# Optimization experiments

Measured on AMD Instinct MI355X. Metric: run time of the kernel, lower is better.

Reference implementation:

```python
import jax, jax.numpy as jnp
import numpy as np

B = 64        # graphs per batch
H = 8         # heads
EH = 16       # each_head = ceil(128/8)
HD = 128      # h_dimension
N_DA = 100000
N_Q = 20000
E_DA = 1000000
E_Q = 200000
EPS = 1e-5    # BatchNorm1d eps
SLOPE = 2.0   # leaky_relu_GAT_rate


def setup_inputs() -> dict:
    key = jax.random.key(0)
    ks = jax.random.split(key, 24)
    r = lambda i, shape, s=1.0: jax.random.normal(ks[i], shape, dtype=jnp.float32) * s
    return {
        'h_da_last': r(0, (N_DA, HD)),
        'h_q_last': r(1, (N_Q, HD)),
        'h_da_0': r(2, (N_DA, HD)),
        'h_q_0': r(3, (N_Q, HD)),
        'W_L': r(4, (HD, HD), 0.05), 'b_L': jnp.zeros((HD,), jnp.float32),
        'gateq_W': r(5, (HD, 1), 0.05), 'gateq_b': jnp.zeros((1,), jnp.float32),
        'gate1_W': r(6, (HD, 1), 0.05), 'gate1_b': jnp.zeros((1,), jnp.float32),
        'gate2_W': r(7, (HD, 1), 0.05), 'gate2_b': jnp.zeros((1,), jnp.float32),
        'Q_comb': r(8, (1, HD), 0.1),
        'Qf_W1': r(9, (HD, 2 * HD), 0.05), 'Qf_b1': jnp.zeros((2 * HD,), jnp.float32),
        'Qf_W2': r(10, (2 * HD, 2 * H * EH), 0.05), 'Qf_b2': jnp.zeros((2 * H * EH,), jnp.float32),
        'end_W1': r(11, (H * EH, 2 * HD), 0.05), 'end_b1': jnp.zeros((2 * HD,), jnp.float32),
        'end_W2': r(12, (2 * HD, HD), 0.05), 'end_b2': jnp.zeros((HD,), jnp.float32),
        'src_da': jax.random.randint(ks[13], (E_DA,), 0, N_DA),
        'dst_da': jax.random.randint(ks[14], (E_DA,), 0, N_DA),
        'src_q': jax.random.randint(ks[15], (E_Q,), 0, N_Q),
        'dst_q': jax.random.randint(ks[16], (E_Q,), 0, N_Q),
        'gid_da': jnp.sort(jax.random.randint(ks[17], (N_DA,), 0, B)),
        'gid_q': jnp.sort(jax.random.randint(ks[18], (N_Q,), 0, B)),
        'PEid': jax.random.randint(ks[19], (100000,), 0, E_DA),
        'DEid': jax.random.randint(ks[20], (100000,), 0, E_DA),
        'len_Mn': 5,
    }


def _bn(y):
    # BatchNorm1d(affine=False), training mode: biased batch stats
    mu = jnp.mean(y, axis=0)
    var = jnp.mean((y - mu) ** 2, axis=0)
    return (y - mu) / jnp.sqrt(var + EPS)


def _fnn(x, W1, b1, W2, b2):
    y = jax.nn.elu(_bn(x @ W1 + b1))
    return jax.nn.elu(_bn(y @ W2 + b2))


def _gap(W, b, feat, gid):
    # GlobalAttentionPooling: softmax(gate) over nodes per graph, weighted sum
    g = (feat @ W + b)[:, 0]                               # [N]
    m = jax.ops.segment_max(g, gid, num_segments=B)
    e = jnp.exp(g - m[gid])
    s = jax.ops.segment_sum(e, gid, num_segments=B)
    w = e / s[gid]
    return jax.ops.segment_sum(w[:, None] * feat, gid, num_segments=B)  # [B, HD]


def _edge_softmax(e, dst, n):
    # softmax over incoming edges per destination node, per head. e: [E, H, 1]
    m = jax.ops.segment_max(e, dst, num_segments=n)
    ex = jnp.exp(e - m[dst])
    s = jax.ops.segment_sum(ex, dst, num_segments=n)
    return ex / s[dst]


def forward(h_da_last, h_q_last, h_da_0, h_q_0, W_L, b_L, gateq_W, gateq_b,
            gate1_W, gate1_b, gate2_W, gate2_b, Q_comb, Qf_W1, Qf_b1, Qf_W2, Qf_b2,
            end_W1, end_b1, end_W2, end_b2,
            src_da, dst_da, src_q, dst_q, gid_da, gid_q, PEid, DEid, len_Mn):
    tmp_q = h_q_last  # MM is None branch

    # graph-level query representation -> per-graph attention queries Q [B, H, 2*EH]
    glq = _gap(gateq_W, gateq_b, h_q_last, gid_q)
    Q = _fnn(glq, Qf_W1, Qf_b1, Qf_W2, Qf_b2).reshape(B, H, 2 * EH)

    def att_comb(M1, M2, gid):
        # ATTpolling_for_3Dtensor with shared Q_comb
        k1 = _gap(gate1_W, gate1_b, M1, gid)
        k2 = _gap(gate2_W, gate2_b, M2, gid)
        s = jnp.stack([(Q_comb * k1).sum(-1), (Q_comb * k2).sum(-1)], axis=-1)  # [B, 2]
        a = jax.nn.softmax(s, axis=-1)[gid]                                     # [N, 2]
        return M1 * a[:, 0:1] + M2 * a[:, 1:2]

    def branch(h_last, tmp, h0, M2, src, dst, gid, n):
        Qn = Q[gid]                                  # [n, H, 2*EH]
        Ql, Qr = Qn[..., :EH], Qn[..., EH:]
        feat = (tmp @ W_L + b_L).reshape(n, H, EH)
        el = (feat * Ql).sum(-1, keepdims=True)      # [n, H, 1]
        er = (feat * Qr).sum(-1, keepdims=True)
        fh = att_comb(h0, M2, gid)
        ft = (fh @ W_L + b_L).reshape(n, H, EH)
        e = jax.nn.leaky_relu(el[src] + er[dst], negative_slope=SLOPE)  # [E, H, 1]
        a = _edge_softmax(e, dst, n)
        agg = jax.ops.segment_sum(ft[src] * a, dst, num_segments=n)     # [n, H, EH]
        out = _fnn(agg.reshape(n, H * EH), end_W1, end_b1, end_W2, end_b2)
        return h_last + out, a                       # residual=True

    h_q_next, _ = branch(h_q_last, tmp_q, h_q_0, h_q_last + (h_q_last - tmp_q),
                         src_q, dst_q, gid_q, N_Q)
    h_da_next, a_da = branch(h_da_last, h_da_last, h_da_0, h_da_last,
                             src_da, dst_da, gid_da, N_DA)

    PE = a_da[PEid].sum(axis=0)                      # [H, 1]
    DE = a_da[DEid].sum(axis=0)
    loss = -1.0 * jnp.mean((PE - DE) / len_Mn, axis=0).reshape(1, 1)
    return h_da_next, h_q_next, loss


def reference(h_da_last, h_q_last, h_da_0, h_q_0, W_L, b_L, gateq_W, gateq_b,
              gate1_W, gate1_b, gate2_W, gate2_b, Q_comb, Qf_W1, Qf_b1, Qf_W2, Qf_b2,
              end_W1, end_b1, end_W2, end_b2,
              src_da, dst_da, src_q, dst_q, gid_da, gid_q, PEid, DEid, len_Mn):
    return forward(h_da_last, h_q_last, h_da_0, h_q_0, W_L, b_L, gateq_W, gateq_b,
                   gate1_W, gate1_b, gate2_W, gate2_b, Q_comb, Qf_W1, Qf_b1, Qf_W2, Qf_b2,
                   end_W1, end_b1, end_W2, end_b2,
                   src_da, dst_da, src_q, dst_q, gid_da, gid_q, PEid, DEid, len_Mn)
```

## Files before the change

### kernel.cpp

```cpp
#include <hip/hip_runtime.h>
#include <math.h>

static constexpr int CB   = 64;
static constexpr int CH   = 8;
static constexpr int CEH  = 16;
static constexpr int CHD  = 128;
static constexpr int CNDA = 100000;
static constexpr int CNQ  = 20000;
static constexpr int CEDA = 1000000;
static constexpr int CEQ  = 200000;
static constexpr float CEPS = 1e-5f;
static constexpr float CSLOPE = 2.0f;

typedef unsigned short ushortt;
typedef __attribute__((ext_vector_type(8))) short bf16x8;
typedef __attribute__((ext_vector_type(4))) float f32x4;

__device__ __forceinline__ float ldf(const float* p) { return *p; }
__device__ __forceinline__ float ldf(const ushortt* p) {
  return __uint_as_float(((unsigned)*p) << 16);
}
__device__ __forceinline__ void stf(float* p, float v) { *p = v; }
__device__ __forceinline__ void stf(ushortt* p, float v) {
  unsigned u = __float_as_uint(v);
  u += 0x7fff + ((u >> 16) & 1);
  *p = (ushortt)(u >> 16);
}
__device__ __forceinline__ short f2bf(float v) {
  unsigned u = __float_as_uint(v);
  u += 0x7fff + ((u >> 16) & 1);
  return (short)(u >> 16);
}
__device__ __forceinline__ float bf2f(short b) {
  return __uint_as_float(((unsigned)(ushortt)b) << 16);
}
__device__ __forceinline__ unsigned fenc(float f) {
  unsigned b = __float_as_uint(f);
  return (b & 0x80000000u) ? ~b : (b | 0x80000000u);
}
__device__ __forceinline__ float fdec(unsigned u) {
  unsigned b = (u & 0x80000000u) ? (u ^ 0x80000000u) : ~u;
  return __uint_as_float(b);
}

__global__ void k_zero(float* __restrict__ p, long n) {
  long i = (long)blockIdx.x * blockDim.x + threadIdx.x;
  long stride = (long)gridDim.x * blockDim.x;
  for (; i < n; i += stride) p[i] = 0.f;
}
static inline void zero_launch(void* p, long n, hipStream_t s) {
  long b = (n + 255) / 256;
  int blocks = (int)(b > 4096 ? 4096 : (b < 1 ? 1 : b));
  hipLaunchKernelGGL(k_zero, dim3(blocks), dim3(256), 0, s, (float*)p, n);
}

__global__ void k_binit(int* start, int n) {
  int i = threadIdx.x;
  if (i <= CB) start[i] = n;
}
__global__ void k_bmark(const int* __restrict__ gid, int n, int* __restrict__ start) {
  int i = blockIdx.x * blockDim.x + threadIdx.x;
  if (i >= n) return;
  int g = gid[i];
  if (i == 0 || gid[i - 1] != g) atomicMin(&start[g], i);
}
__global__ void k_bfix(int* start) {
  if (threadIdx.x == 0) {
    for (int g = CB - 1; g >= 0; --g)
      if (start[g] > start[g + 1]) start[g] = start[g + 1];
  }
}

__global__ void k_gate_dot(const float* __restrict__ feat, const float* __restrict__ gw,
                           const float* __restrict__ gb, float* __restrict__ g, int n) {
  int wave = (blockIdx.x * blockDim.x + threadIdx.x) >> 6;
  int lane = threadIdx.x & 63;
  if (wave >= n) return;
  const float* row = feat + (size_t)wave * CHD;
  float v = row[lane] * gw[lane] + row[lane + 64] * gw[lane + 64];
  for (int off = 32; off > 0; off >>= 1) v += __shfl_down(v, off, 64);
  if (lane == 0) g[wave] = v + gb[0];
}

__global__ void k_gate_dot2(const float* __restrict__ feat,
                            const float* __restrict__ w1, const float* __restrict__ b1,
                            const float* __restrict__ w2, const float* __restrict__ b2,
                            float* __restrict__ g1, float* __restrict__ g2, int n) {
  int wave = (blockIdx.x * blockDim.x + threadIdx.x) >> 6;
  int lane = threadIdx.x & 63;
  if (wave >= n) return;
  const float* row = feat + (size_t)wave * CHD;
  float r0 = row[lane], r1 = row[lane + 64];
  float v1 = r0 * w1[lane] + r1 * w1[lane + 64];
  float v2 = r0 * w2[lane] + r1 * w2[lane + 64];
  for (int off = 32; off > 0; off >>= 1) {
    v1 += __shfl_down(v1, off, 64);
    v2 += __shfl_down(v2, off, 64);
  }
  if (lane == 0) {
    g1[wave] = v1 + b1[0];
    g2[wave] = v2 + b2[0];
  }
}

__global__ void k_gmax5(const float* __restrict__ gq, const int* __restrict__ startq,
                        const int* __restrict__ startda, float* __restrict__ m) {
  int job = blockIdx.x >> 6, grp = blockIdx.x & 63;
  const float* g;
  const int* start;
  if (job == 0)      { g = gq;                              start = startq; }
  else if (job == 1) { g = gq + 2 * (size_t)CNQ;            start = startq; }
  else if (job == 2) { g = gq + (size_t)CNQ;                start = startq; }
  else if (job == 3) { g = gq + 3 * (size_t)CNQ;            start = startda; }
  else               { g = gq + 3 * (size_t)CNQ + CNDA;     start = startda; }
  int s0 = start[grp], s1 = start[grp + 1];
  int t = threadIdx.x;
  __shared__ float red[256];
  float v = -1e30f;
  for (int i = s0 + t; i < s1; i += 256) v = fmaxf(v, g[i]);
  red[t] = v;
  __syncthreads();
  for (int o = 128; o > 0; o >>= 1) {
    if (t < o) red[t] = fmaxf(red[t], red[t + o]);
    __syncthreads();
  }
  if (t == 0) m[job * 64 + grp] = red[0];
}

template <int NG>
__global__ __launch_bounds__(128) void k_gap_partial(
    const float* __restrict__ g0, const float* __restrict__ g1,
    const float* __restrict__ feat, const int* __restrict__ start,
    const float* __restrict__ m,
    float* __restrict__ acc0, float* __restrict__ acc1,
    float* __restrict__ sums) {
  int grp = blockIdx.x;
  int s0 = start[grp], s1 = start[grp + 1];
  int len = s1 - s0;
  if (len <= 0) return;
  int NC = gridDim.y;
  int per = (len + NC - 1) / NC;
  int r0 = s0 + blockIdx.y * per;
  int r1 = min(s1, r0 + per);
  if (r0 >= r1) return;
  int t = threadIdx.x;
  float m0 = m[grp];
  float m1 = (NG == 2) ? m[64 + grp] : 0.f;
  float a0 = 0.f, a1 = 0.f, sum0 = 0.f, sum1 = 0.f;
  for (int i = r0; i < r1; ++i) {
    float f = feat[(size_t)i * CHD + t];
    float e0 = __expf(g0[i] - m0);
    sum0 += e0;
    a0 += e0 * f;
    if (NG == 2) {
      float e1 = __expf(g1[i] - m1);
      sum1 += e1;
      a1 += e1 * f;
    }
  }
  atomicAdd(&acc0[grp * CHD + t], a0);
  if (NG == 2) atomicAdd(&acc1[grp * CHD + t], a1);
  if (t == 0) {
    atomicAdd(&sums[grp], sum0);
    if (NG == 2) atomicAdd(&sums[64 + grp], sum1);
  }
}

__global__ void k_gap_norm5(float* __restrict__ glq, const float* __restrict__ sbuf) {
  int job = blockIdx.x >> 6, grp = blockIdx.x & 63;
  int t = threadIdx.x;
  int smap = (job == 1) ? 2 : ((job == 2) ? 1 : job);
  float sv = sbuf[smap * 64 + grp];
  float* acc = glq + (size_t)job * CB * CHD + grp * CHD;
  float v = acc[t];
  acc[t] = (sv > 0.f) ? v / sv : 0.f;
}

__global__ void k_mm_small(const float* __restrict__ X, const float* __restrict__ W,
                           const float* __restrict__ bias, float* __restrict__ Y,
                           int m, int k, int p) {
  int idx = blockIdx.x * blockDim.x + threadIdx.x;
  if (idx >= m * p) return;
  int r = idx / p, c = idx % p;
  const float* xr = X + (size_t)r * k;
  const float* wc = W + c;
  float acc = bias[c];
  int kk = 0;
  for (; kk + 8 <= k; kk += 8) {
    float xv[8], wv[8];
#pragma unroll
    for (int j = 0; j < 8; ++j) {
      xv[j] = xr[kk + j];
      wv[j] = wc[(size_t)(kk + j) * p];
    }
#pragma unroll
    for (int j = 0; j < 8; ++j) acc += xv[j] * wv[j];
  }
  for (; kk < k; ++kk) acc += xr[kk] * wc[(size_t)kk * p];
  Y[idx] = acc;
}

__global__ void k_bn_elu_small(float* __restrict__ Y, int m, int p) {
  int c = blockIdx.x * blockDim.x + threadIdx.x;
  if (c >= p) return;
  float s = 0.f, s2 = 0.f;
  int i = 0;
  for (; i + 8 <= m; i += 8) {
    float v[8];
#pragma unroll
    for (int j = 0; j < 8; ++j) v[j] = Y[(size_t)(i + j) * p + c];
#pragma unroll
    for (int j = 0; j < 8; ++j) { s += v[j]; s2 += v[j] * v[j]; }
  }
  for (; i < m; ++i) {
    float v = Y[(size_t)i * p + c];
    s += v; s2 += v * v;
  }
  float mu = s / m;
  float var = s2 / m - mu * mu;
  float inv = rsqrtf(var + CEPS);
  i = 0;
  for (; i + 8 <= m; i += 8) {
    float v[8];
#pragma unroll
    for (int j = 0; j < 8; ++j) v[j] = Y[(size_t)(i + j) * p + c];
#pragma unroll
    for (int j = 0; j < 8; ++j) {
      float x = (v[j] - mu) * inv;
      Y[(size_t)(i + j) * p + c] = x > 0.f ? x : expm1f(x);
    }
  }
  for (; i < m; ++i) {
    float x = (Y[(size_t)i * p + c] - mu) * inv;
    Y[(size_t)i * p + c] = x > 0.f ? x : expm1f(x);
  }
}

__global__ void k_attcomb(const float* __restrict__ k1, const float* __restrict__ k2,
                          const float* __restrict__ Qc, float* __restrict__ a) {
  int grp = blockIdx.x;
  int t = threadIdx.x;
  float v1 = Qc[t] * k1[grp * CHD + t] + Qc[t + 64] * k1[grp * CHD + t + 64];
  float v2 = Qc[t] * k2[grp * CHD + t] + Qc[t + 64] * k2[grp * CHD + t + 64];
  for (int off = 32; off > 0; off >>= 1) {
    v1 += __shfl_down(v1, off, 64);
    v2 += __shfl_down(v2, off, 64);
  }
  if (t == 0) {
    float mx = fmaxf(v1, v2);
    float e1 = expf(v1 - mx), e2 = expf(v2 - mx);
    float s = e1 + e2;
    a[grp * 2] = e1 / s;
    a[grp * 2 + 1] = e2 / s;
  }
}

__global__ void k_wq(const float* __restrict__ W_L, const float* __restrict__ b_L,
                     const float* __restrict__ Qm, float* __restrict__ WQ,
                     float* __restrict__ bQ) {
  int g = blockIdx.x;
  int t = threadIdx.x;
  for (int j = 0; j < 8; ++j) {
    int idx = t + j * 256;
    int d = idx >> 4, c = idx & 15;
    int h = c & 7, off = (c >= 8) ? CEH : 0;
    const float* w = W_L + d * CHD + h * CEH;
    const float* q = Qm + g * 256 + h * 32 + off;
    float acc = 0.f;
#pragma unroll
    for (int e = 0; e < CEH; ++e) acc += w[e] * q[e];
    WQ[g * 2048 + idx] = acc;
  }
  if (t < 16) {
    int c = t, h = c & 7, off = (c >= 8) ? CEH : 0;
    const float* b = b_L + h * CEH;
    const float* q = Qm + g * 256 + h * 32 + off;
    float acc = 0.f;
#pragma unroll
    for (int e = 0; e < CEH; ++e) acc += b[e] * q[e];
    bQ[g * 16 + c] = acc;
  }
}

__global__ void k_eler(const float* __restrict__ tmp, const float* __restrict__ WQ,
                       const float* __restrict__ bQ, const int* __restrict__ gid,
                       float* __restrict__ elr, int n) {
  int idx = blockIdx.x * blockDim.x + threadIdx.x;
  if (idx >= n * 16) return;
  int i = idx >> 4, c = idx & 15;
  int g = gid[i];
  const float* wq = WQ + g * 2048 + c;
  const float* row = tmp + (size_t)i * CHD;
  float acc = bQ[g * 16 + c];
#pragma unroll 4
  for (int d = 0; d < CHD; ++d) acc += row[d] * wq[d * 16];
  elr[idx] = acc;
}

__global__ void k_elmax(const float* __restrict__ elr, unsigned* __restrict__ mgl, int n) {
  int h = blockIdx.x;
  int chunk = blockIdx.y;
  int per = (n + 31) / 32;
  int i0 = chunk * per, i1 = min(n, i0 + per);
  int t = threadIdx.x;
  __shared__ float red[256];
  float v = -1e30f;
  for (int i = i0 + t; i < i1; i += 256) v = fmaxf(v, elr[(size_t)i * 16 + h]);
  red[t] = v;
  __syncthreads();
  for (int o = 128; o > 0; o >>= 1) {
    if (t < o) red[t] = fmaxf(red[t], red[t + o]);
    __syncthreads();
  }
  if (t == 0) atomicMax(&mgl[h], fenc(red[0]));
}

__global__ void k_tcast(const float* __restrict__ W, ushortt* __restrict__ WT,
                        int K, int P) {
  int i = blockIdx.x * blockDim.x + threadIdx.x;
  if (i >= K * P) return;
  int p = i / K, k = i % K;
  stf(&WT[i], W[(size_t)k * P + p]);
}

template <int P>
__global__ void k_bn_prep(const float* __restrict__ stats, float* __restrict__ pr, int n) {
  int c = threadIdx.x;
  if (c >= P) return;
  float invn = 1.f / (float)n;
  float mu = stats[c] * invn;
  float var = stats[P + c] * invn - mu * mu;
  pr[c] = mu;
  pr[P + c] = rsqrtf(var + CEPS);
}

template <int TP>
__global__ void k_stats_reduce(const float* __restrict__ pstat, float* __restrict__ stats,
                               int nb) {
  int c = blockIdx.x * blockDim.x + threadIdx.x;
  if (c >= TP) return;
  int NC = gridDim.y;
  int per = (nb + NC - 1) / NC;
  int r0 = blockIdx.y * per;
  int r1 = min(nb, r0 + per);
  if (r0 >= r1) return;
  float s0 = 0.f, s1 = 0.f, s2 = 0.f, s3 = 0.f;
  int r = r0;
  for (; r + 4 <= r1; r += 4) {
    s0 += pstat[(size_t)(r + 0) * TP + c];
    s1 += pstat[(size_t)(r + 1) * TP + c];
    s2 += pstat[(size_t)(r + 2) * TP + c];
    s3 += pstat[(size_t)(r + 3) * TP + c];
  }
  for (; r < r1; ++r) s0 += pstat[(size_t)r * TP + c];
  atomicAdd(&stats[c], (s0 + s1) + (s2 + s3));
}

template <int K, int P, int XM, bool STATS, typename OT>
__global__ __launch_bounds__(256, 2) void k_gemm_mfma(
    const void* __restrict__ X0v, const void* __restrict__ X1v,
    const float* __restrict__ acomb, const int* __restrict__ gid,
    const float* __restrict__ bnmu, const float* __restrict__ bninv,
    const ushortt* __restrict__ BT, const float* __restrict__ bias,
    OT* __restrict__ Y, float* __restrict__ pstat, int n) {
  constexpr int NT = P / 16;
  const int wave = threadIdx.x >> 6, lane = threadIdx.x & 63;
  const int quad = lane >> 4, l16 = lane & 15;
  const int r0w = blockIdx.x * 64 + wave * 16;
  const int rA = r0w + l16;
  const bool rowok = rA < n;
  f32x4 acc[NT];
#pragma unroll
  for (int t = 0; t < NT; ++t) acc[t] = f32x4{0.f, 0.f, 0.f, 0.f};
  float a0 = 0.f, a1 = 0.f;
  if (XM == 1 && rowok) {
    int g = gid[rA];
    a0 = acomb[2 * g];
    a1 = acomb[2 * g + 1];
  }
  for (int k0 = 0; k0 < K; k0 += 32) {
    const int kk = k0 + quad * 8;
    bf16x8 af = {};
    if (rowok) {
      if constexpr (XM == 2) {
        af = *(const bf16x8*)((const ushortt*)X0v + (size_t)rA * K + kk);
      } else if constexpr (XM == 3) {
        bf16x8 raw = *(const bf16x8*)((const ushortt*)X0v + (size_t)rA * K + kk);
#pragma unroll
        for (int j = 0; j < 8; ++j) {
          float v = bf2f(raw[j]);
          v = (v - bnmu[kk + j]) * bninv[kk + j];
          v = v > 0.f ? v : (__expf(v) - 1.f);
          af[j] = f2bf(v);
        }
      } else {
        const float* px = (const float*)X0v + (size_t)rA * K + kk;
        float v[8];
        if constexpr (XM == 1) {
          const float* py = (const float*)X1v + (size_t)rA * K + kk;
#pragma unroll
          for (int j = 0; j < 8; ++j) v[j] = a0 * px[j] + a1 * py[j];
        } else {
#pragma unroll
          for (int j = 0; j < 8; ++j) v[j] = px[j];
        }
#pragma unroll
        for (int j = 0; j < 8; ++j) af[j] = f2bf(v[j]);
      }
    }
    bf16x8 bfr[NT];
#pragma unroll
    for (int t = 0; t < NT; ++t)
      bfr[t] = *(const bf16x8*)(BT + (size_t)(t * 16 + l16) * K + kk);
#pragma unroll
    for (int t = 0; t < NT; ++t)
      acc[t] = __builtin_amdgcn_mfma_f32_16x16x32_bf16(af, bfr[t], acc[t], 0, 0, 0);
  }
  float* pw = STATS ? (pstat + ((size_t)blockIdx.x * 4 + wave) * (2 * P)) : nullptr;
#pragma unroll
  for (int t = 0; t < NT; ++t) {
    const int c = t * 16 + l16;
    float b = bias[c];
    float s = 0.f, s2 = 0.f;
#pragma unroll
    for (int r = 0; r < 4; ++r) {
      int gr = r0w + quad * 4 + r;
      if (gr < n) {
        float val = acc[t][r] + b;
        stf(Y + (size_t)gr * P + c, val);
        if constexpr (STATS) {
          float vq = (sizeof(OT) == 2) ? bf2f(f2bf(val)) : val;
          s += vq;
          s2 += vq * vq;
        }
      }
    }
    if constexpr (STATS) {
      s += __shfl_xor(s, 16, 64);
      s += __shfl_xor(s, 32, 64);
      s2 += __shfl_xor(s2, 16, 64);
      s2 += __shfl_xor(s2, 32, 64);
      if (quad == 0) {
        pw[c] = s;
        pw[P + c] = s2;
      }
    }
  }
}

__global__ void k_count(const int* __restrict__ dst, int* __restrict__ counts, int E) {
  int e = blockIdx.x * blockDim.x + threadIdx.x;
  if (e < E) atomicAdd(&counts[dst[e]], 1);
}
__global__ void k_scan_reduce(const int* __restrict__ counts, int* __restrict__ bsum, int n) {
  __shared__ int red[256];
  int t = threadIdx.x;
  int base = blockIdx.x * 1024;
  int s = 0;
  for (int j = 0; j < 4; ++j) {
    int i = base + t * 4 + j;
    if (i < n) s += counts[i];
  }
  red[t] = s;
  __syncthreads();
  for (int o = 128; o > 0; o >>= 1) {
    if (t < o) red[t] += red[t + o];
    __syncthreads();
  }
  if (t == 0) bsum[blockIdx.x] = red[0];
}
__global__ void k_scan_top(int* __restrict__ bsum, int nb) {
  __shared__ int sh[128];
  int t = threadIdx.x;
  int v = (t < nb) ? bsum[t] : 0;
  sh[t] = v;
  __syncthreads();
  for (int o = 1; o < 128; o <<= 1) {
    int x = (t >= o) ? sh[t - o] : 0;
    __syncthreads();
    sh[t] += x;
    __syncthreads();
  }
  if (t < nb) bsum[t] = sh[t] - v;
}
__global__ void k_scan_final(const int* __restrict__ counts, const int* __restrict__ bsum,
                             int* __restrict__ rowptr, int n, int E) {
  __shared__ int sh[256];
  int t = threadIdx.x;
  int base = blockIdx.x * 1024;
  int v[4];
  int s = 0;
  for (int j = 0; j < 4; ++j) {
    int i = base + t * 4 + j;
    v[j] = (i < n) ? counts[i] : 0;
    s += v[j];
  }
  sh[t] = s;
  __syncthreads();
  for (int o = 1; o < 256; o <<= 1) {
    int x = (t >= o) ? sh[t - o] : 0;
    __syncthreads();
    sh[t] += x;
    __syncthreads();
  }
  int off = bsum[blockIdx.x] + sh[t] - s;
  for (int j = 0; j < 4; ++j) {
    int i = base + t * 4 + j;
    if (i < n) rowptr[i] = off;
    off += v[j];
  }
  if (blockIdx.x == 0 && t == 0) rowptr[n] = E;
}
__global__ void k_copy_int(const int* __restrict__ a, int* __restrict__ b, int n) {
  int i = blockIdx.x * blockDim.x + threadIdx.x;
  if (i < n) b[i] = a[i];
}
__global__ void k_scatter(const int* __restrict__ dst, const int* __restrict__ srcA,
                          int* __restrict__ cursor, int* __restrict__ csr_src, int E) {
  int e = blockIdx.x * blockDim.x + threadIdx.x;
  if (e >= E) return;
  int d = dst[e];
  int pos = atomicAdd(&cursor[d], 1);
  csr_src[pos] = srcA[e];
}

__global__ __launch_bounds__(256) void k_node_agg(
    const int* __restrict__ rowptr, const int* __restrict__ csr_src,
    const float* __restrict__ elr, const unsigned* __restrict__ mgl,
    const ushortt* __restrict__ ft,
    float* __restrict__ agg, float* __restrict__ mOut, float* __restrict__ sOut, int n) {
  int node = blockIdx.x * 4 + (threadIdx.x >> 6);
  if (node >= n) return;
  int lane = threadIdx.x & 63;
  int h_p = lane & 7;
  int e_loc = lane >> 3;
  int h_a = lane >> 3;
  int s0 = rowptr[node], s1 = rowptr[node + 1];
  if (s1 <= s0) {
    *(float2*)(agg + (size_t)node * CHD + lane * 2) = make_float2(0.f, 0.f);
    if (lane < 8) {
      mOut[(size_t)node * CH + lane] = -1e30f;
      sOut[(size_t)node * CH + lane] = 0.f;
    }
    return;
  }
  float erd_p = elr[(size_t)node * 16 + 8 + h_p];
  float xm = fdec(mgl[h_p]) + erd_p;
  float m_p = xm >= 0.f ? xm : CSLOPE * xm;
  float s_part = 0.f, a0 = 0.f, a1 = 0.f;
  for (int base = s0; base < s1; base += 8) {
    int cnt = s1 - base;
    int sj = 0;
    float p = 0.f;
    if (e_loc < cnt) {
      sj = csr_src[base + e_loc];
      float x = elr[(size_t)sj * 16 + h_p] + erd_p;
      x = x >= 0.f ? x : CSLOPE * x;
      p = __expf(x - m_p);
      s_part += p;
    }
#pragma unroll
    for (int e = 0; e < 8; ++e) {
      float pe = __shfl(p, e * 8 + h_a, 64);
      int se = __shfl(sj, e * 8, 64);
      unsigned ftv = *(const unsigned*)(ft + (size_t)se * CHD + lane * 2);
      a0 += pe * __uint_as_float(ftv << 16);
      a1 += pe * __uint_as_float(ftv & 0xffff0000u);
    }
  }
  s_part += __shfl_xor(s_part, 8, 64);
  s_part += __shfl_xor(s_part, 16, 64);
  s_part += __shfl_xor(s_part, 32, 64);
  float s_acc = __shfl(s_part, h_a, 64);
  float inv = 1.f / s_acc;
  float2 o;
  o.x = a0 * inv;
  o.y = a1 * inv;
  *(float2*)(agg + (size_t)node * CHD + lane * 2) = o;
  if (lane < 8) {
    mOut[(size_t)node * CH + lane] = m_p;
    sOut[(size_t)node * CH + lane] = s_part;
  }
}

__global__ void k_bn_apply_f4(float* __restrict__ Y, const float* __restrict__ stats,
                              const float* __restrict__ hlast, int n) {
  int idx = blockIdx.x * blockDim.x + threadIdx.x;
  if (idx >= n * 32) return;
  int cg = (idx & 31) * 4;
  float invn = 1.f / (float)n;
  float4 y = ((const float4*)Y)[idx];
  float4 hl = ((const float4*)hlast)[idx];
  float yy[4] = {y.x, y.y, y.z, y.w};
  float hh[4] = {hl.x, hl.y, hl.z, hl.w};
  float o[4];
#pragma unroll
  for (int j = 0; j < 4; ++j) {
    float mu = stats[cg + j] * invn;
    float var = stats[128 + cg + j] * invn - mu * mu;
    float v = (yy[j] - mu) * rsqrtf(var + CEPS);
    v = v > 0.f ? v : (__expf(v) - 1.f);
    o[j] = v + hh[j];
  }
  ((float4*)Y)[idx] = make_float4(o[0], o[1], o[2], o[3]);
}

__device__ __forceinline__ float attn_val(int e, int h, const int* __restrict__ src,
                                          const int* __restrict__ dst,
                                          const float* __restrict__ elr,
                                          const float* __restrict__ mOut,
                                          const float* __restrict__ sOut) {
  int ss = src[e], sd = dst[e];
  float x = elr[(size_t)ss * 16 + h] + elr[(size_t)sd * 16 + 8 + h];
  x = x >= 0.f ? x : CSLOPE * x;
  return __expf(x - mOut[(size_t)sd * CH + h]) / sOut[(size_t)sd * CH + h];
}

__global__ void k_pd(const int* __restrict__ src, const int* __restrict__ dst,
                     const float* __restrict__ elr, const float* __restrict__ mOut,
                     const float* __restrict__ sOut, const int* __restrict__ PEid,
                     const int* __restrict__ DEid, float* __restrict__ pdp,
                     int nPE, int nDE) {
  __shared__ float part[CH];
  if (threadIdx.x < CH) part[threadIdx.x] = 0.f;
  __syncthreads();
  int idx = blockIdx.x * blockDim.x + threadIdx.x;
  int j = idx >> 3, h = idx & 7;
  float acc = 0.f;
  if (j < nPE) acc += attn_val(PEid[j], h, src, dst, elr, mOut, sOut);
  if (j < nDE) acc -= attn_val(DEid[j], h, src, dst, elr, mOut, sOut);
  atomicAdd(&part[h], acc);
  __syncthreads();
  if (threadIdx.x < CH) pdp[(size_t)blockIdx.x * CH + threadIdx.x] = part[threadIdx.x];
}
__global__ void k_loss(const float* __restrict__ pdp, int nb,
                       const int* __restrict__ lenMn, float* __restrict__ out) {
  __shared__ float part[CH];
  int t = threadIdx.x;
  if (t < CH) part[t] = 0.f;
  __syncthreads();
  int h = t & 7;
  float acc = 0.f;
  for (int j = t >> 3; j < nb; j += 32) acc += pdp[(size_t)j * CH + h];
  atomicAdd(&part[h], acc);
  __syncthreads();
  if (t == 0) {
    float len = (float)lenMn[0];
    float s = 0.f;
    for (int hh = 0; hh < CH; ++hh) s += part[hh] / len;
    out[0] = -s / (float)CH;
  }
}

static void run_branch(int n, int E, const float* h_last, const float* h0,
                       const int* src, const int* dst, const int* gid,
                       const float* acomb, const float* WQ, const float* bQ,
                       const ushortt* W_LT, const float* b_L,
                       const ushortt* W1T, const float* end_b1,
                       const ushortt* W2T, const float* end_b2,
                       float* U, float* elr, unsigned* mgl, float* mOut, float* sOut,
                       int* counts, int* rowptr, int* cursor, int* csr_src, int* bsum,
                       float* stats ,
                       float* bnpr , float* pstat, float* out, hipStream_t stream) {
  ushortt* ftB = (ushortt*)U;
  ushortt* y1B = (ushortt*)U;
  float* stats1 = stats;
  float* stats2 = stats + 512;
  int nChunks = (n + 1023) / 1024;
  int nbG = (n + 63) / 64;
  int nbW = nbG * 4;
  zero_launch(counts, n, stream);
  zero_launch(stats, 1024, stream);
  zero_launch(mgl, 8, stream);
  hipLaunchKernelGGL(k_count, dim3((E + 255) / 256), dim3(256), 0, stream, dst, counts, E);
  hipLaunchKernelGGL(k_scan_reduce, dim3(nChunks), dim3(256), 0, stream, counts, bsum, n);
  hipLaunchKernelGGL(k_scan_top, dim3(1), dim3(128), 0, stream, bsum, nChunks);
  hipLaunchKernelGGL(k_scan_final, dim3(nChunks), dim3(256), 0, stream, counts, bsum, rowptr, n, E);
  hipLaunchKernelGGL(k_copy_int, dim3((n + 255) / 256), dim3(256), 0, stream, rowptr, cursor, n);
  hipLaunchKernelGGL(k_scatter, dim3((E + 255) / 256), dim3(256), 0, stream, dst, src, cursor, csr_src, E);
  hipLaunchKernelGGL(k_eler, dim3((n * 16 + 255) / 256), dim3(256), 0, stream,
                     h_last, WQ, bQ, gid, elr, n);
  hipLaunchKernelGGL(k_elmax, dim3(8, 32), dim3(256), 0, stream, elr, mgl, n);
  hipLaunchKernelGGL((k_gemm_mfma<128, 128, 1, false, ushortt>), dim3(nbG),
                     dim3(256), 0, stream, h0, h_last, acomb, gid,
                     (const float*)nullptr, (const float*)nullptr,
                     W_LT, b_L, ftB, (float*)nullptr, n);
  hipLaunchKernelGGL(k_node_agg, dim3((n + 3) / 4), dim3(256), 0, stream,
                     rowptr, csr_src, elr, mgl, ftB, out, mOut, sOut, n);
  hipLaunchKernelGGL((k_gemm_mfma<128, 256, 0, true, ushortt>), dim3(nbG),
                     dim3(256), 0, stream, out, (const void*)nullptr,
                     (const float*)nullptr, (const int*)nullptr,
                     (const float*)nullptr, (const float*)nullptr,
                     W1T, end_b1, y1B, pstat, n);
  hipLaunchKernelGGL((k_stats_reduce<512>), dim3(2, 64), dim3(256), 0, stream,
                     pstat, stats1, nbW);
  hipLaunchKernelGGL((k_bn_prep<256>), dim3(1), dim3(256), 0, stream, stats1, bnpr, n);
  hipLaunchKernelGGL((k_gemm_mfma<256, 128, 3, true, float>), dim3(nbG),
                     dim3(256), 0, stream, y1B, (const void*)nullptr,
                     (const float*)nullptr, (const int*)nullptr,
                     bnpr, bnpr + 256,
                     W2T, end_b2, out, pstat, n);
  hipLaunchKernelGGL((k_stats_reduce<256>), dim3(1, 64), dim3(256), 0, stream,
                     pstat, stats2, nbW);
  hipLaunchKernelGGL(k_bn_apply_f4, dim3((n * 32 + 255) / 256), dim3(256), 0, stream,
                     out, stats2, h_last, n);
}

extern "C" void kernel_launch(void* const* d_in, const int* in_sizes, int n_in,
                              void* d_out, int out_size, void* d_ws, size_t ws_size,
                              hipStream_t stream) {
  const float* h_da_last = (const float*)d_in[0];
  const float* h_q_last  = (const float*)d_in[1];
  const float* h_da_0    = (const float*)d_in[2];
  const float* h_q_0     = (const float*)d_in[3];
  const float* W_L       = (const float*)d_in[4];
  const float* b_L       = (const float*)d_in[5];
  const float* gateq_W   = (const float*)d_in[6];
  const float* gateq_b   = (const float*)d_in[7];
  const float* gate1_W   = (const float*)d_in[8];
  const float* gate1_b   = (const float*)d_in[9];
  const float* gate2_W   = (const float*)d_in[10];
  const float* gate2_b   = (const float*)d_in[11];
  const float* Q_comb    = (const float*)d_in[12];
  const float* Qf_W1     = (const float*)d_in[13];
  const float* Qf_b1     = (const float*)d_in[14];
  const float* Qf_W2     = (const float*)d_in[15];
  const float* Qf_b2     = (const float*)d_in[16];
  const float* end_W1    = (const float*)d_in[17];
  const float* end_b1    = (const float*)d_in[18];
  const float* end_W2    = (const float*)d_in[19];
  const float* end_b2    = (const float*)d_in[20];
  const int* src_da = (const int*)d_in[21];
  const int* dst_da = (const int*)d_in[22];
  const int* src_q  = (const int*)d_in[23];
  const int* dst_q  = (const int*)d_in[24];
  const int* gid_da = (const int*)d_in[25];
  const int* gid_q  = (const int*)d_in[26];
  const int* PEid   = (const int*)d_in[27];
  const int* DEid   = (const int*)d_in[28];
  const int* len_Mn = (const int*)d_in[29];

  float* out_da   = (float*)d_out;
  float* out_q    = (float*)d_out + (size_t)CNDA * CHD;
  float* out_loss = (float*)d_out + (size_t)CNDA * CHD + (size_t)CNQ * CHD;

  float* ws = (float*)d_ws;
  size_t off = 0;
  auto alloc = [&](size_t cnt) { float* p = ws + off; off += cnt; return p; };
  float* U    = alloc((size_t)CNDA * 128);
  float* elr  = alloc((size_t)CNDA * 16);
  float* mOut = alloc((size_t)CNDA * CH);
  float* sOut = alloc((size_t)CNDA * CH);
  int* counts  = (int*)alloc(CNDA);
  int* rowptr  = (int*)alloc(CNDA + 4);
  int* cursor  = (int*)alloc(CNDA);
  int* csr_src = (int*)alloc(CEDA);
  int* bsum    = (int*)alloc(128);
  ushortt* W_LT = (ushortt*)alloc(128 * 128 / 2);
  ushortt* W1T  = (ushortt*)alloc(128 * 256 / 2);
  ushortt* W2T  = (ushortt*)alloc(256 * 128 / 2);
  float* WQ   = alloc((size_t)CB * 2048);
  float* bQ   = alloc((size_t)CB * 16);
  float* gq   = alloc(CNQ);
  float* g1q  = alloc(CNQ);
  float* g2q  = alloc(CNQ);
  float* g1da = alloc(CNDA);
  float* g2da = alloc(CNDA);
  float* glq  = alloc(CB * CHD);
  float* k1q  = alloc(CB * CHD);
  float* k2q  = alloc(CB * CHD);
  float* k1da = alloc(CB * CHD);
  float* k2da = alloc(CB * CHD);
  float* Qt   = alloc(CB * 256);
  float* Qm   = alloc(CB * 256);
  float* acq  = alloc(CB * 2);
  float* acda = alloc(CB * 2);
  float* stats = alloc(1024);
  float* bnpr  = alloc(512);
  unsigned* mgl = (unsigned*)alloc(8);
  float* mbuf  = alloc(5 * 64);
  float* sbuf  = alloc(5 * 64);
  int* startq  = (int*)alloc(68);
  int* startda = (int*)alloc(68);
  float* pstat = alloc(((size_t)(CNDA + 63) / 64) * 4 * 512);
  float* pdp   = alloc(((size_t)CNDA * CH + 255) / 256 * CH);
  (void)ws_size; (void)n_in; (void)out_size;

  hipLaunchKernelGGL(k_tcast, dim3((128 * 128 + 255) / 256), dim3(256), 0, stream, W_L, W_LT, 128, 128);
  hipLaunchKernelGGL(k_tcast, dim3((128 * 256 + 255) / 256), dim3(256), 0, stream, end_W1, W1T, 128, 256);
  hipLaunchKernelGGL(k_tcast, dim3((256 * 128 + 255) / 256), dim3(256), 0, stream, end_W2, W2T, 256, 128);

  hipLaunchKernelGGL(k_binit, dim3(1), dim3(128), 0, stream, startq, CNQ);
  hipLaunchKernelGGL(k_binit, dim3(1), dim3(128), 0, stream, startda, CNDA);
  hipLaunchKernelGGL(k_bmark, dim3((CNQ + 255) / 256), dim3(256), 0, stream, gid_q, CNQ, startq);
  hipLaunchKernelGGL(k_bmark, dim3((CNDA + 255) / 256), dim3(256), 0, stream, gid_da, CNDA, startda);
  hipLaunchKernelGGL(k_bfix, dim3(1), dim3(64), 0, stream, startq);
  hipLaunchKernelGGL(k_bfix, dim3(1), dim3(64), 0, stream, startda);

  hipLaunchKernelGGL(k_gate_dot2, dim3((CNQ + 3) / 4), dim3(256), 0, stream,
                     h_q_last, gateq_W, gateq_b, gate2_W, gate2_b, gq, g2q, CNQ);
  hipLaunchKernelGGL(k_gate_dot, dim3((CNQ + 3) / 4), dim3(256), 0, stream, h_q_0, gate1_W, gate1_b, g1q, CNQ);
  hipLaunchKernelGGL(k_gate_dot, dim3((CNDA + 3) / 4), dim3(256), 0, stream, h_da_0, gate1_W, gate1_b, g1da, CNDA);
  hipLaunchKernelGGL(k_gate_dot, dim3((CNDA + 3) / 4), dim3(256), 0, stream, h_da_last, gate2_W, gate2_b, g2da, CNDA);

  hipLaunchKernelGGL(k_gmax5, dim3(5 * CB), dim3(256), 0, stream, gq, startq, startda, mbuf);
  zero_launch(glq, 5 * (size_t)CB * CHD, stream);
  zero_launch(sbuf, 5 * 64, stream);
  hipLaunchKernelGGL((k_gap_partial<2>), dim3(CB, 32), dim3(128), 0, stream,
                     gq, g2q, h_q_last, startq, mbuf + 0, glq, k2q, sbuf + 0);
  hipLaunchKernelGGL((k_gap_partial<1>), dim3(CB, 32), dim3(128), 0, stream,
                     g1q, (const float*)nullptr, h_q_0, startq, mbuf + 128,
                     k1q, (float*)nullptr, sbuf + 128);
  hipLaunchKernelGGL((k_gap_partial<1>), dim3(CB, 32), dim3(128), 0, stream,
                     g1da, (const float*)nullptr, h_da_0, startda, mbuf + 192,
                     k1da, (float*)nullptr, sbuf + 192);
  hipLaunchKernelGGL((k_gap_partial<1>), dim3(CB, 32), dim3(128), 0, stream,
                     g2da, (const float*)nullptr, h_da_last, startda, mbuf + 256,
                     k2da, (float*)nullptr, sbuf + 256);
  hipLaunchKernelGGL(k_gap_norm5, dim3(5 * CB), dim3(128), 0, stream, glq, sbuf);

  hipLaunchKernelGGL(k_mm_small, dim3((CB * 256 + 255) / 256), dim3(256), 0, stream,
                     glq, Qf_W1, Qf_b1, Qt, CB, 128, 256);
  hipLaunchKernelGGL(k_bn_elu_small, dim3(1), dim3(256), 0, stream, Qt, CB, 256);
  hipLaunchKernelGGL(k_mm_small, dim3((CB * 256 + 255) / 256), dim3(256), 0, stream,
                     Qt, Qf_W2, Qf_b2, Qm, CB, 256, 256);
  hipLaunchKernelGGL(k_bn_elu_small, dim3(1), dim3(256), 0, stream, Qm, CB, 256);

  hipLaunchKernelGGL(k_wq, dim3(CB), dim3(256), 0, stream, W_L, b_L, Qm, WQ, bQ);

  hipLaunchKernelGGL(k_attcomb, dim3(CB), dim3(64), 0, stream, k1q, k2q, Q_comb, acq);
  hipLaunchKernelGGL(k_attcomb, dim3(CB), dim3(64), 0, stream, k1da, k2da, Q_comb, acda);

  run_branch(CNQ, CEQ, h_q_last, h_q_0, src_q, dst_q, gid_q, acq, WQ, bQ,
             W_LT, b_L, W1T, end_b1, W2T, end_b2,
             U, elr, mgl, mOut, sOut, counts, rowptr, cursor, csr_src, bsum,
             stats, bnpr, pstat, out_q, stream);

  run_branch(CNDA, CEDA, h_da_last, h_da_0, src_da, dst_da, gid_da, acda, WQ, bQ,
             W_LT, b_L, W1T, end_b1, W2T, end_b2,
             U, elr, mgl, mOut, sOut, counts, rowptr, cursor, csr_src, bsum,
             stats, bnpr, pstat, out_da, stream);

  int nPE = in_sizes[27], nDE = in_sizes[28];
  int nMax = nPE > nDE ? nPE : nDE;
  int nbPD = (nMax * CH + 255) / 256;
  hipLaunchKernelGGL(k_pd, dim3(nbPD), dim3(256), 0, stream,
                     src_da, dst_da, elr, mOut, sOut, PEid, DEid, pdp, nPE, nDE);
  hipLaunchKernelGGL(k_loss, dim3(1), dim3(256), 0, stream, pdp, nbPD, len_Mn, out_loss);
}
```

Measured before the change: 1.102 ms.

## Add multi-row register tiling and LDS-staged swizzled weights to MFMA GEMM

The MFMA GEMM kernel gains a ROWS template parameter, so each wave computes several 16-row tiles and reuses each loaded B fragment across them. The W_L and end_W2 GEMMs now use two row tiles per wave. An LDSB option stages the whole transposed weight matrix in shared memory with an XOR swizzle to avoid bank conflicts, and it is used for the W1 GEMM. BN mean and inverse-std parameters are also cached in LDS. In exchange, the kernel uses more registers, which may lower occupancy, and launches fewer blocks.

```diff
diff --git a/kernel.cpp b/kernel.cpp
--- a/kernel.cpp
+++ b/kernel.cpp
@@ -356,82 +356,121 @@
   atomicAdd(&stats[c], (s0 + s1) + (s2 + s3));
 }
 
-template <int K, int P, int XM, bool STATS, typename OT>
+template <int K, int P, int XM, bool STATS, int ROWS, bool LDSB, typename OT>
 __global__ __launch_bounds__(256, 2) void k_gemm_mfma(
     const void* __restrict__ X0v, const void* __restrict__ X1v,
     const float* __restrict__ acomb, const int* __restrict__ gid,
-    const float* __restrict__ bnmu, const float* __restrict__ bninv,
-    const ushortt* __restrict__ BT, const float* __restrict__ bias,
-    OT* __restrict__ Y, float* __restrict__ pstat, int n) {
+    const float* __restrict__ bnpr, const ushortt* __restrict__ BT,
+    const float* __restrict__ bias, OT* __restrict__ Y,
+    float* __restrict__ pstat, int n) {
   constexpr int NT = P / 16;
+  __shared__ ushortt sB[LDSB ? P * K : 1];
+  __shared__ float sbn[(XM == 3) ? 2 * K : 1];
+  if constexpr (XM == 3) {
+    for (int i = threadIdx.x; i < 2 * K; i += 256) sbn[i] = bnpr[i];
+  }
+  if constexpr (LDSB) {
+    for (int i = threadIdx.x; i < P * (K / 8); i += 256) {
+      int row = i / (K / 8), seg = i % (K / 8);
+      int sseg = seg ^ (row & 7);
+      *(bf16x8*)&sB[row * K + sseg * 8] =
+          *(const bf16x8*)(BT + (size_t)row * K + seg * 8);
+    }
+  }
+  if constexpr (XM == 3 || LDSB) __syncthreads();
   const int wave = threadIdx.x >> 6, lane = threadIdx.x & 63;
   const int quad = lane >> 4, l16 = lane & 15;
-  const int r0w = blockIdx.x * 64 + wave * 16;
-  const int rA = r0w + l16;
-  const bool rowok = rA < n;
-  f32x4 acc[NT];
-#pragma unroll
-  for (int t = 0; t < NT; ++t) acc[t] = f32x4{0.f, 0.f, 0.f, 0.f};
-  float a0 = 0.f, a1 = 0.f;
-  if (XM == 1 && rowok) {
-    int g = gid[rA];
-    a0 = acomb[2 * g];
-    a1 = acomb[2 * g + 1];
-  }
+  const int rbase = blockIdx.x * (64 * ROWS) + wave * 16;
+  int rA[ROWS];
+  bool rok[ROWS];
+  float a0[ROWS], a1[ROWS];
+#pragma unroll
+  for (int rr = 0; rr < ROWS; ++rr) {
+    rA[rr] = rbase + rr * 64 + l16;
+    rok[rr] = rA[rr] < n;
+    a0[rr] = 0.f; a1[rr] = 0.f;
+    if (XM == 1 && rok[rr]) {
+      int g = gid[rA[rr]];
+      a0[rr] = acomb[2 * g];
+      a1[rr] = acomb[2 * g + 1];
+    }
+  }
+  f32x4 acc[ROWS][NT];
+#pragma unroll
+  for (int rr = 0; rr < ROWS; ++rr)
+#pragma unroll
+    for (int t = 0; t < NT; ++t) acc[rr][t] = f32x4{0.f, 0.f, 0.f, 0.f};
   for (int k0 = 0; k0 < K; k0 += 32) {
     const int kk = k0 + quad * 8;
-    bf16x8 af = {};
-    if (rowok) {
-      if constexpr (XM == 2) {
-        af = *(const bf16x8*)((const ushortt*)X0v + (size_t)rA * K + kk);
-      } else if constexpr (XM == 3) {
-        bf16x8 raw = *(const bf16x8*)((const ushortt*)X0v + (size_t)rA * K + kk);
-#pragma unroll
-        for (int j = 0; j < 8; ++j) {
-          float v = bf2f(raw[j]);
-          v = (v - bnmu[kk + j]) * bninv[kk + j];
-          v = v > 0.f ? v : (__expf(v) - 1.f);
-          af[j] = f2bf(v);
+    bf16x8 af[ROWS];
+#pragma unroll
+    for (int rr = 0; rr < ROWS; ++rr) {
+      af[rr] = bf16x8{};
+      if (rok[rr]) {
+        if constexpr (XM == 2) {
+          af[rr] = *(const bf16x8*)((const ushortt*)X0v + (size_t)rA[rr] * K + kk);
+        } else if constexpr (XM == 3) {
+          bf16x8 raw = *(const bf16x8*)((const ushortt*)X0v + (size_t)rA[rr] * K + kk);
+#pragma unroll
+          for (int j = 0; j < 8; ++j) {
+            float v = bf2f(raw[j]);
+            v = (v - sbn[kk + j]) * sbn[K + kk + j];
+            v = v > 0.f ? v : (__expf(v) - 1.f);
+            af[rr][j] = f2bf(v);
+          }
+        } else {
+          const float* px = (const float*)X0v + (size_t)rA[rr] * K + kk;
+          float v[8];
+          if constexpr (XM == 1) {
+            const float* py = (const float*)X1v + (size_t)rA[rr] * K + kk;
+#pragma unroll
+            for (int j = 0; j < 8; ++j) v[j] = a0[rr] * px[j] + a1[rr] * py[j];
+          } else {
+#pragma unroll
+            for (int j = 0; j < 8; ++j) v[j] = px[j];
+          }
+#pragma unroll
+          for (int j = 0; j < 8; ++j) af[rr][j] = f2bf(v[j]);
         }
+      }
+    }
+    bf16x8 bfr[NT];
+#pragma unroll
+    for (int t = 0; t < NT; ++t) {
+      if constexpr (LDSB) {
+        int row = t * 16 + l16;
+        int sseg = (kk >> 3) ^ (row & 7);
+        bfr[t] = *(const bf16x8*)&sB[row * K + sseg * 8];
       } else {
-        const float* px = (const float*)X0v + (size_t)rA * K + kk;
-        float v[8];
-        if constexpr (XM == 1) {
-          const float* py = (const float*)X1v + (size_t)rA * K + kk;
-#pragma unroll
-          for (int j = 0; j < 8; ++j) v[j] = a0 * px[j] + a1 * py[j];
-        } else {
-#pragma unroll
-          for (int j = 0; j < 8; ++j) v[j] = px[j];
-        }
-#pragma unroll
-        for (int j = 0; j < 8; ++j) af[j] = f2bf(v[j]);
+        bfr[t] = *(const bf16x8*)(BT + (size_t)(t * 16 + l16) * K + kk);
       }
     }
-    bf16x8 bfr[NT];
-#pragma unroll
-    for (int t = 0; t < NT; ++t)
-      bfr[t] = *(const bf16x8*)(BT + (size_t)(t * 16 + l16) * K + kk);
-#pragma unroll
-    for (int t = 0; t < NT; ++t)
-      acc[t] = __builtin_amdgcn_mfma_f32_16x16x32_bf16(af, bfr[t], acc[t], 0, 0, 0);
-  }
-  float* pw = STATS ? (pstat + ((size_t)blockIdx.x * 4 + wave) * (2 * P)) : nullptr;
+#pragma unroll
+    for (int rr = 0; rr < ROWS; ++rr)
+#pragma unroll
+      for (int t = 0; t < NT; ++t)
+        acc[rr][t] = __builtin_amdgcn_mfma_f32_16x16x32_bf16(af[rr], bfr[t], acc[rr][t], 0, 0, 0);
+  }
+  float* pw = nullptr;
+  if constexpr (STATS) pw = pstat + ((size_t)blockIdx.x * 4 + wave) * (2 * P);
 #pragma unroll
   for (int t = 0; t < NT; ++t) {
     const int c = t * 16 + l16;
     float b = bias[c];
     float s = 0.f, s2 = 0.f;
 #pragma unroll
-    for (int r = 0; r < 4; ++r) {
-      int gr = r0w + quad * 4 + r;
-      if (gr < n) {
-        float val = acc[t][r] + b;
-        stf(Y + (size_t)gr * P + c, val);
-        if constexpr (STATS) {
-          float vq = (sizeof(OT) == 2) ? bf2f(f2bf(val)) : val;
-          s += vq;
-          s2 += vq * vq;
+    for (int rr = 0; rr < ROWS; ++rr) {
+#pragma unroll
+      for (int r = 0; r < 4; ++r) {
+        int gr = rbase + rr * 64 + quad * 4 + r;
+        if (gr < n) {
+          float val = acc[rr][t][r] + b;
+          stf(Y + (size_t)gr * P + c, val);
+          if constexpr (STATS) {
+            float vq = (sizeof(OT) == 2) ? bf2f(f2bf(val)) : val;
+            s += vq;
+            s2 += vq * vq;
+          }
         }
       }
     }
@@ -667,8 +706,8 @@
   float* stats1 = stats;
   float* stats2 = stats + 512;
   int nChunks = (n + 1023) / 1024;
-  int nbG = (n + 63) / 64;
-  int nbW = nbG * 4;
+  int nbG1 = (n + 127) / 128;
+  int nbG2 = (n + 63) / 64;
   zero_launch(counts, n, stream);
   zero_launch(stats, 1024, stream);
   zero_launch(mgl, 8, stream);
@@ -681,27 +720,24 @@
   hipLaunchKernelGGL(k_eler, dim3((n * 16 + 255) / 256), dim3(256), 0, stream,
                      h_last, WQ, bQ, gid, elr, n);
   hipLaunchKernelGGL(k_elmax, dim3(8, 32), dim3(256), 0, stream, elr, mgl, n);
-  hipLaunchKernelGGL((k_gemm_mfma<128, 128, 1, false, ushortt>), dim3(nbG),
+  hipLaunchKernelGGL((k_gemm_mfma<128, 128, 1, false, 2, false, ushortt>), dim3(nbG1),
                      dim3(256), 0, stream, h0, h_last, acomb, gid,
-                     (const float*)nullptr, (const float*)nullptr,
-                     W_LT, b_L, ftB, (float*)nullptr, n);
+                     (const float*)nullptr, W_LT, b_L, ftB, (float*)nullptr, n);
   hipLaunchKernelGGL(k_node_agg, dim3((n + 3) / 4), dim3(256), 0, stream,
                      rowptr, csr_src, elr, mgl, ftB, out, mOut, sOut, n);
-  hipLaunchKernelGGL((k_gemm_mfma<128, 256, 0, true, ushortt>), dim3(nbG),
+  hipLaunchKernelGGL((k_gemm_mfma<128, 256, 0, true, 1, true, ushortt>), dim3(nbG2),
                      dim3(256), 0, stream, out, (const void*)nullptr,
                      (const float*)nullptr, (const int*)nullptr,
-                     (const float*)nullptr, (const float*)nullptr,
-                     W1T, end_b1, y1B, pstat, n);
+                     (const float*)nullptr, W1T, end_b1, y1B, pstat, n);
   hipLaunchKernelGGL((k_stats_reduce<512>), dim3(2, 64), dim3(256), 0, stream,
-                     pstat, stats1, nbW);
+                     pstat, stats1, nbG2 * 4);
   hipLaunchKernelGGL((k_bn_prep<256>), dim3(1), dim3(256), 0, stream, stats1, bnpr, n);
-  hipLaunchKernelGGL((k_gemm_mfma<256, 128, 3, true, float>), dim3(nbG),
+  hipLaunchKernelGGL((k_gemm_mfma<256, 128, 3, true, 2, false, float>), dim3(nbG1),
                      dim3(256), 0, stream, y1B, (const void*)nullptr,
                      (const float*)nullptr, (const int*)nullptr,
-                     bnpr, bnpr + 256,
-                     W2T, end_b2, out, pstat, n);
+                     bnpr, W2T, end_b2, out, pstat, n);
   hipLaunchKernelGGL((k_stats_reduce<256>), dim3(1, 64), dim3(256), 0, stream,
-                     pstat, stats2, nbW);
+                     pstat, stats2, nbG1 * 4);
   hipLaunchKernelGGL(k_bn_apply_f4, dim3((n * 32 + 255) / 256), dim3(256), 0, stream,
                      out, stats2, h_last, n);
 }
```

After: 1.070 ms. 1.03x faster.
